# Performance work log

Measured on AMD Instinct MI355X. Metric: run time of the kernel, lower is better.

## Reference

```python
import jax, jax.numpy as jnp
import numpy as np

B, L, E = 256, 500, 300  # bsz, max_doc_len, word_embed_dim
KS = [3, 5, 7]           # filters_size


def setup_inputs() -> dict:
    key = jax.random.key(0)
    ks = jax.random.split(key, 1 + 2 * len(KS))
    inp = {"x": jax.random.normal(ks[0], (B, L, E), jnp.float32)}
    i = 1
    for k in KS:
        # PyTorch Conv2d default init scale ~ 1/sqrt(fan_in)
        inp[f"aw{k}"] = jax.random.normal(ks[i], (k, E), jnp.float32) / np.sqrt(k * E).astype(np.float32); i += 1
        inp[f"ab{k}"] = jnp.zeros((1,), jnp.float32)
        inp[f"cw{k}"] = jax.random.normal(ks[i], (E,), jnp.float32) / np.sqrt(E).astype(np.float32); i += 1
        inp[f"cb{k}"] = jnpp = jnp.zeros((1,), jnp.float32)
    return inp


def _branch(x, aw, ab, cw, cb):
    # x: (B, L, E); aw: (k, E); cw: (E,)
    k = aw.shape[0]
    p = (k - 1) // 2
    x4 = x[:, None, :, :]            # NCHW: (B, 1, L, E)
    w4 = aw[None, None, :, :]        # OIHW: (1, 1, k, E)
    s = jax.lax.conv_general_dilated(x4, w4, window_strides=(1, 1),
                                     padding=((p, p), (0, 0)))  # (B, 1, L, 1)
    score = jax.nn.sigmoid(s + ab[0])[:, 0, :, :]               # (B, L, 1)
    gated = x * score                                           # broadcast over E
    # Conv2d(1,1,(1,E)) == per-timestep dot product over E
    return jnp.tanh(jnp.einsum('ble,e->bl', gated, cw) + cb[0])  # (B, L)


def reference(x, aw3, ab3, cw3, cb3, aw5, ab5, cw5, cb5, aw7, ab7, cw7, cb7):
    return (_branch(x, aw3, ab3, cw3, cb3),
            _branch(x, aw5, ab5, cw5, cb5),
            _branch(x, aw7, ab7, cw7, cb7))
```

## Files before the change

### kernel.cpp

```cpp
#include <hip/hip_runtime.h>
#include <math.h>

#define BB 256
#define LL 500
#define EE 300
#define NROWS (BB * LL)
#define NJ 18
#define NC 75
#define TOUT 56
#define NTILE 9
#define DROWS 64

__global__ __launch_bounds__(256) void fused_kernel(
    const float* __restrict__ x,
    const float* __restrict__ aw3, const float* __restrict__ ab3,
    const float* __restrict__ cw3, const float* __restrict__ cb3,
    const float* __restrict__ aw5, const float* __restrict__ ab5,
    const float* __restrict__ cw5, const float* __restrict__ cb5,
    const float* __restrict__ aw7, const float* __restrict__ ab7,
    const float* __restrict__ cw7, const float* __restrict__ cb7,
    float* __restrict__ out)
{
    __shared__ float4 wlds[NJ * NC];
    __shared__ float dlds[DROWS][NJ + 1];

    const int tid = threadIdx.x;

    {
        const float4* s3a = (const float4*)aw3;
        const float4* s3c = (const float4*)cw3;
        const float4* s5a = (const float4*)aw5;
        const float4* s5c = (const float4*)cw5;
        const float4* s7a = (const float4*)aw7;
        const float4* s7c = (const float4*)cw7;
        for (int i = tid; i < 225; i += 256) wlds[i]        = s3a[i];
        for (int i = tid; i < 75;  i += 256) wlds[225 + i]  = s3c[i];
        for (int i = tid; i < 375; i += 256) wlds[300 + i]  = s5a[i];
        for (int i = tid; i < 75;  i += 256) wlds[675 + i]  = s5c[i];
        for (int i = tid; i < 525; i += 256) wlds[750 + i]  = s7a[i];
        for (int i = tid; i < 75;  i += 256) wlds[1275 + i] = s7c[i];
    }

    const int b    = blockIdx.x / NTILE;
    const int t    = blockIdx.x % NTILE;
    const int l0   = t * TOUT - 3;
    const int wave = tid >> 6;
    const int lane = tid & 63;
    const int g    = lane >> 4;
    const int j    = lane & 15;
    const int lr   = wave * 16 + g * 4;

    bool valid[4];
    const float4* xr[4];
#pragma unroll
    for (int rr = 0; rr < 4; ++rr) {
        const int l = l0 + lr + rr;
        valid[rr] = (l >= 0) && (l < LL);
        const int lc = l < 0 ? 0 : (l >= LL ? LL - 1 : l);
        xr[rr] = (const float4*)(x + ((size_t)b * LL + lc) * EE);
    }

    float4 xall[5][4];
#pragma unroll
    for (int k = 0; k < 5; ++k) {
        const int c = (k == 4) ? ((j < 11) ? (j + 64) : 74) : (j + 16 * k);
#pragma unroll
        for (int rr = 0; rr < 4; ++rr) xall[k][rr] = xr[rr][c];
    }

    __syncthreads();

    float acc[NJ][4];
#pragma unroll
    for (int d = 0; d < NJ; ++d)
#pragma unroll
        for (int rr = 0; rr < 4; ++rr) acc[d][rr] = 0.0f;

#define COMPUTE(k, c)                                                               \
    {                                                                               \
        _Pragma("unroll")                                                           \
        for (int d = 0; d < NJ; ++d) {                                              \
            const float4 w = wlds[d * NC + (c)];                                    \
            acc[d][0] = fmaf(xall[k][0].w, w.w, fmaf(xall[k][0].z, w.z, fmaf(xall[k][0].y, w.y, fmaf(xall[k][0].x, w.x, acc[d][0])))); \
            acc[d][1] = fmaf(xall[k][1].w, w.w, fmaf(xall[k][1].z, w.z, fmaf(xall[k][1].y, w.y, fmaf(xall[k][1].x, w.x, acc[d][1])))); \
            acc[d][2] = fmaf(xall[k][2].w, w.w, fmaf(xall[k][2].z, w.z, fmaf(xall[k][2].y, w.y, fmaf(xall[k][2].x, w.x, acc[d][2])))); \
            acc[d][3] = fmaf(xall[k][3].w, w.w, fmaf(xall[k][3].z, w.z, fmaf(xall[k][3].y, w.y, fmaf(xall[k][3].x, w.x, acc[d][3])))); \
        }                                                                           \
    }

    COMPUTE(0, j)
    COMPUTE(1, j + 16)
    COMPUTE(2, j + 32)
    COMPUTE(3, j + 48)
    if (j < 11) {
        COMPUTE(4, j + 64)
    }
#undef COMPUTE

#pragma unroll
    for (int d = 0; d < NJ; ++d)
#pragma unroll
        for (int rr = 0; rr < 4; ++rr) {
            float v = acc[d][rr];
            v += __shfl_xor(v, 1, 16);
            v += __shfl_xor(v, 2, 16);
            v += __shfl_xor(v, 4, 16);
            v += __shfl_xor(v, 8, 16);
            acc[d][rr] = v;
        }

#pragma unroll
    for (int rr = 0; rr < 4; ++rr) {
        if (j == rr) {
            const float vf = valid[rr] ? 1.0f : 0.0f;
#pragma unroll
            for (int d = 0; d < NJ; ++d) dlds[lr + rr][d] = acc[d][rr] * vf;
        }
    }

    __syncthreads();

    if (wave < 3 && lane < TOUT) {
        const int lo = t * TOUT + lane;
        if (lo < LL) {
            const int c = lane + 3;
            const int r = b * LL + lo;

            if (wave == 0) {
                float pre = 0.0f;
#pragma unroll
                for (int tp = 0; tp < 3; ++tp) pre += dlds[c + tp - 1][tp];
                const float s = 1.0f / (1.0f + expf(-(pre + ab3[0])));
                out[r] = tanhf(s * dlds[c][3] + cb3[0]);
            } else if (wave == 1) {
                float pre = 0.0f;
#pragma unroll
                for (int tp = 0; tp < 5; ++tp) pre += dlds[c + tp - 2][4 + tp];
                const float s = 1.0f / (1.0f + expf(-(pre + ab5[0])));
                out[NROWS + r] = tanhf(s * dlds[c][9] + cb5[0]);
            } else {
                float pre = 0.0f;
#pragma unroll
                for (int tp = 0; tp < 7; ++tp) pre += dlds[c + tp - 3][10 + tp];
                const float s = 1.0f / (1.0f + expf(-(pre + ab7[0])));
                out[2 * NROWS + r] = tanhf(s * dlds[c][17] + cb7[0]);
            }
        }
    }
}

extern "C" void kernel_launch(void* const* d_in, const int* in_sizes, int n_in,
                              void* d_out, int out_size, void* d_ws, size_t ws_size,
                              hipStream_t stream) {
    const float* x   = (const float*)d_in[0];
    const float* aw3 = (const float*)d_in[1];
    const float* ab3 = (const float*)d_in[2];
    const float* cw3 = (const float*)d_in[3];
    const float* cb3 = (const float*)d_in[4];
    const float* aw5 = (const float*)d_in[5];
    const float* ab5 = (const float*)d_in[6];
    const float* cw5 = (const float*)d_in[7];
    const float* cb5 = (const float*)d_in[8];
    const float* aw7 = (const float*)d_in[9];
    const float* ab7 = (const float*)d_in[10];
    const float* cw7 = (const float*)d_in[11];
    const float* cb7 = (const float*)d_in[12];

    float* out = (float*)d_out;

    fused_kernel<<<BB * NTILE, 256, 0, stream>>>(
        x, aw3, ab3, cw3, cb3, aw5, ab5, cw5, cb5, aw7, ab7, cw7, cb7, out);
}
```

Measured before the change: 258.4 us.

## Stage x through double-buffered LDS in E-chunks with larger row tiles

Replaces the per-block register load of a 56-row tile with a 250-row tile per block (2 blocks per batch). x is streamed through a double-buffered shared-memory buffer in 5-float4 E-chunks, with the next chunk prefetched into registers while the current one is computed. Each thread now accumulates 9 dot products for 2 rows directly, which removes the cross-lane shuffle reductions and cuts halo reloads from 9 tiles to 2. The cost is a grid of only 512 blocks and a barrier on every chunk iteration.

```diff
diff --git a/kernel.cpp b/kernel.cpp
--- a/kernel.cpp
+++ b/kernel.cpp
@@ -7,9 +7,11 @@
 #define NROWS (BB * LL)
 #define NJ 18
 #define NC 75
-#define TOUT 56
-#define NTILE 9
-#define DROWS 64
+#define CB 5
+#define NB 15
+#define DR 256
+#define TOUT 250
+#define XB4 (DR * CB)
 
 __global__ __launch_bounds__(256) void fused_kernel(
     const float* __restrict__ x,
@@ -22,9 +24,28 @@
     float* __restrict__ out)
 {
     __shared__ float4 wlds[NJ * NC];
-    __shared__ float dlds[DROWS][NJ + 1];
+    __shared__ float4 xbuf[2][XB4];
+    float* dlds = (float*)&xbuf[0][0];
 
     const int tid = threadIdx.x;
+    const int b   = blockIdx.x >> 1;
+    const int t   = blockIdx.x & 1;
+    const int l0  = t * TOUT - 3;
+
+    const float4* xp[5];
+#pragma unroll
+    for (int q = 0; q < 5; ++q) {
+        const int L   = q * 256 + tid;
+        const int row = L / CB;
+        const int cc  = L - row * CB;
+        int g = l0 + row;
+        g = g < 0 ? 0 : (g >= LL ? LL - 1 : g);
+        xp[q] = (const float4*)(x + ((size_t)b * LL + g) * EE) + cc;
+    }
+
+    float4 xn[5];
+#pragma unroll
+    for (int q = 0; q < 5; ++q) xn[q] = xp[q][0];
 
     {
         const float4* s3a = (const float4*)aw3;
@@ -41,110 +62,83 @@
         for (int i = tid; i < 75;  i += 256) wlds[1275 + i] = s7c[i];
     }
 
-    const int b    = blockIdx.x / NTILE;
-    const int t    = blockIdx.x % NTILE;
-    const int l0   = t * TOUT - 3;
-    const int wave = tid >> 6;
-    const int lane = tid & 63;
-    const int g    = lane >> 4;
-    const int j    = lane & 15;
-    const int lr   = wave * 16 + g * 4;
-
-    bool valid[4];
-    const float4* xr[4];
 #pragma unroll
-    for (int rr = 0; rr < 4; ++rr) {
-        const int l = l0 + lr + rr;
-        valid[rr] = (l >= 0) && (l < LL);
-        const int lc = l < 0 ? 0 : (l >= LL ? LL - 1 : l);
-        xr[rr] = (const float4*)(x + ((size_t)b * LL + lc) * EE);
-    }
-
-    float4 xall[5][4];
-#pragma unroll
-    for (int k = 0; k < 5; ++k) {
-        const int c = (k == 4) ? ((j < 11) ? (j + 64) : 74) : (j + 16 * k);
-#pragma unroll
-        for (int rr = 0; rr < 4; ++rr) xall[k][rr] = xr[rr][c];
-    }
+    for (int q = 0; q < 5; ++q) xbuf[0][q * 256 + tid] = xn[q];
 
     __syncthreads();
 
-    float acc[NJ][4];
+    const int wav   = tid >> 6;
+    const int lane  = tid & 63;
+    const int dbase = (wav >> 1) * 9;
+    const int rbase = (wav & 1) * 128 + lane;
+
+    float vf0, vf1;
+    { const int g0 = l0 + rbase;      vf0 = (g0 >= 0 && g0 < LL) ? 1.0f : 0.0f; }
+    { const int g1 = l0 + rbase + 64; vf1 = (g1 >= 0 && g1 < LL) ? 1.0f : 0.0f; }
+
+    float acc[9][2];
 #pragma unroll
-    for (int d = 0; d < NJ; ++d)
+    for (int dd = 0; dd < 9; ++dd) { acc[dd][0] = 0.0f; acc[dd][1] = 0.0f; }
+
+#pragma unroll 1
+    for (int s = 0; s < NB; ++s) {
+        if (s < NB - 1) {
 #pragma unroll
-        for (int rr = 0; rr < 4; ++rr) acc[d][rr] = 0.0f;
+            for (int q = 0; q < 5; ++q) { xp[q] += CB; xn[q] = xp[q][0]; }
+        }
 
-#define COMPUTE(k, c)                                                               \
-    {                                                                               \
-        _Pragma("unroll")                                                           \
-        for (int d = 0; d < NJ; ++d) {                                              \
-            const float4 w = wlds[d * NC + (c)];                                    \
-            acc[d][0] = fmaf(xall[k][0].w, w.w, fmaf(xall[k][0].z, w.z, fmaf(xall[k][0].y, w.y, fmaf(xall[k][0].x, w.x, acc[d][0])))); \
-            acc[d][1] = fmaf(xall[k][1].w, w.w, fmaf(xall[k][1].z, w.z, fmaf(xall[k][1].y, w.y, fmaf(xall[k][1].x, w.x, acc[d][1])))); \
-            acc[d][2] = fmaf(xall[k][2].w, w.w, fmaf(xall[k][2].z, w.z, fmaf(xall[k][2].y, w.y, fmaf(xall[k][2].x, w.x, acc[d][2])))); \
-            acc[d][3] = fmaf(xall[k][3].w, w.w, fmaf(xall[k][3].z, w.z, fmaf(xall[k][3].y, w.y, fmaf(xall[k][3].x, w.x, acc[d][3])))); \
-        }                                                                           \
+        const float4* xb = &xbuf[s & 1][rbase * CB];
+        const float4* wb = &wlds[dbase * NC + s * CB];
+
+#pragma unroll
+        for (int cc = 0; cc < CB; ++cc) {
+            const float4 x0 = xb[cc];
+            const float4 x1 = xb[64 * CB + cc];
+#pragma unroll
+            for (int dd = 0; dd < 9; ++dd) {
+                const float4 w = wb[dd * NC + cc];
+                acc[dd][0] = fmaf(x0.w, w.w, fmaf(x0.z, w.z, fmaf(x0.y, w.y, fmaf(x0.x, w.x, acc[dd][0]))));
+                acc[dd][1] = fmaf(x1.w, w.w, fmaf(x1.z, w.z, fmaf(x1.y, w.y, fmaf(x1.x, w.x, acc[dd][1]))));
+            }
+        }
+
+        if (s < NB - 1) {
+#pragma unroll
+            for (int q = 0; q < 5; ++q) xbuf[(s + 1) & 1][q * 256 + tid] = xn[q];
+        }
+        __syncthreads();
     }
 
-    COMPUTE(0, j)
-    COMPUTE(1, j + 16)
-    COMPUTE(2, j + 32)
-    COMPUTE(3, j + 48)
-    if (j < 11) {
-        COMPUTE(4, j + 64)
+#pragma unroll
+    for (int dd = 0; dd < 9; ++dd) {
+        dlds[rbase * (NJ + 1) + dbase + dd]        = acc[dd][0] * vf0;
+        dlds[(rbase + 64) * (NJ + 1) + dbase + dd] = acc[dd][1] * vf1;
     }
-#undef COMPUTE
-
-#pragma unroll
-    for (int d = 0; d < NJ; ++d)
-#pragma unroll
-        for (int rr = 0; rr < 4; ++rr) {
-            float v = acc[d][rr];
-            v += __shfl_xor(v, 1, 16);
-            v += __shfl_xor(v, 2, 16);
-            v += __shfl_xor(v, 4, 16);
-            v += __shfl_xor(v, 8, 16);
-            acc[d][rr] = v;
-        }
-
-#pragma unroll
-    for (int rr = 0; rr < 4; ++rr) {
-        if (j == rr) {
-            const float vf = valid[rr] ? 1.0f : 0.0f;
-#pragma unroll
-            for (int d = 0; d < NJ; ++d) dlds[lr + rr][d] = acc[d][rr] * vf;
-        }
-    }
-
     __syncthreads();
 
-    if (wave < 3 && lane < TOUT) {
-        const int lo = t * TOUT + lane;
-        if (lo < LL) {
-            const int c = lane + 3;
-            const int r = b * LL + lo;
-
-            if (wave == 0) {
-                float pre = 0.0f;
+    if (tid < TOUT) {
+        const int c = tid + 3;
+        const int r = b * LL + t * TOUT + tid;
+        {
+            float pre = 0.0f;
 #pragma unroll
-                for (int tp = 0; tp < 3; ++tp) pre += dlds[c + tp - 1][tp];
-                const float s = 1.0f / (1.0f + expf(-(pre + ab3[0])));
-                out[r] = tanhf(s * dlds[c][3] + cb3[0]);
-            } else if (wave == 1) {
-                float pre = 0.0f;
+            for (int tp = 0; tp < 3; ++tp) pre += dlds[(c + tp - 1) * (NJ + 1) + tp];
+            const float sg = 1.0f / (1.0f + expf(-(pre + ab3[0])));
+            out[r] = tanhf(sg * dlds[c * (NJ + 1) + 3] + cb3[0]);
+        }
+        {
+            float pre = 0.0f;
 #pragma unroll
-                for (int tp = 0; tp < 5; ++tp) pre += dlds[c + tp - 2][4 + tp];
-                const float s = 1.0f / (1.0f + expf(-(pre + ab5[0])));
-                out[NROWS + r] = tanhf(s * dlds[c][9] + cb5[0]);
-            } else {
-                float pre = 0.0f;
+            for (int tp = 0; tp < 5; ++tp) pre += dlds[(c + tp - 2) * (NJ + 1) + 4 + tp];
+            const float sg = 1.0f / (1.0f + expf(-(pre + ab5[0])));
+            out[NROWS + r] = tanhf(sg * dlds[c * (NJ + 1) + 9] + cb5[0]);
+        }
+        {
+            float pre = 0.0f;
 #pragma unroll
-                for (int tp = 0; tp < 7; ++tp) pre += dlds[c + tp - 3][10 + tp];
-                const float s = 1.0f / (1.0f + expf(-(pre + ab7[0])));
-                out[2 * NROWS + r] = tanhf(s * dlds[c][17] + cb7[0]);
-            }
+            for (int tp = 0; tp < 7; ++tp) pre += dlds[(c + tp - 3) * (NJ + 1) + 10 + tp];
+            const float sg = 1.0f / (1.0f + expf(-(pre + ab7[0])));
+            out[2 * NROWS + r] = tanhf(sg * dlds[c * (NJ + 1) + 17] + cb7[0]);
         }
     }
 }
@@ -168,6 +162,6 @@
 
     float* out = (float*)d_out;
 
-    fused_kernel<<<BB * NTILE, 256, 0, stream>>>(
+    fused_kernel<<<BB * 2, 256, 0, stream>>>(
         x, aw3, ab3, cw3, cb3, aw5, ab5, cw5, cb5, aw7, ab7, cw7, cb7, out);
 }
```

Result: slower. 292.3 us (+13.1%).

## Process three tiles per block with register prefetch and DPP reductions

Applied to the files above, without the earlier changes.

Each block now handles three consecutive sequence tiles instead of one, which cuts the grid from 2304 to 768 blocks and loads the weight table into LDS once per three tiles. While the current tile is being reduced and written, the next tile's x rows are prefetched into registers. The shuffle-based 16-lane reduction is replaced with DPP row operations, and custom waitcnt+barrier fences replace __syncthreads. Risks are fewer blocks for latency hiding, higher register pressure from the prefetch, and an extra barrier per tile.

```diff
diff --git a/kernel.cpp b/kernel.cpp
--- a/kernel.cpp
+++ b/kernel.cpp
@@ -8,8 +8,29 @@
 #define NJ 18
 #define NC 75
 #define TOUT 56
-#define NTILE 9
+#define GRP 3
+#define NT 3
 #define DROWS 64
+
+
+__device__ __forceinline__ float red16(float v) {
+    int t;
+    t = __builtin_amdgcn_update_dpp(0, __float_as_int(v), 0xB1, 0xF, 0xF, true);
+    v += __int_as_float(t);
+    t = __builtin_amdgcn_update_dpp(0, __float_as_int(v), 0x4E, 0xF, 0xF, true);
+    v += __int_as_float(t);
+    t = __builtin_amdgcn_update_dpp(0, __float_as_int(v), 0x124, 0xF, 0xF, true);
+    v += __int_as_float(t);
+    t = __builtin_amdgcn_update_dpp(0, __float_as_int(v), 0x128, 0xF, 0xF, true);
+    v += __int_as_float(t);
+    return v;
+}
+
+__device__ __forceinline__ void lds_fence_barrier() {
+    asm volatile("s_waitcnt lgkmcnt(0)" ::: "memory");
+    __builtin_amdgcn_s_barrier();
+    asm volatile("" ::: "memory");
+}
 
 __global__ __launch_bounds__(256) void fused_kernel(
     const float* __restrict__ x,
@@ -41,40 +62,51 @@
         for (int i = tid; i < 75;  i += 256) wlds[1275 + i] = s7c[i];
     }
 
-    const int b    = blockIdx.x / NTILE;
-    const int t    = blockIdx.x % NTILE;
-    const int l0   = t * TOUT - 3;
+    const int b    = blockIdx.x / GRP;
+    const int grp  = blockIdx.x % GRP;
     const int wave = tid >> 6;
     const int lane = tid & 63;
     const int g    = lane >> 4;
     const int j    = lane & 15;
     const int lr   = wave * 16 + g * 4;
 
-    bool valid[4];
-    const float4* xr[4];
-#pragma unroll
-    for (int rr = 0; rr < 4; ++rr) {
-        const int l = l0 + lr + rr;
-        valid[rr] = (l >= 0) && (l < LL);
-        const int lc = l < 0 ? 0 : (l >= LL ? LL - 1 : l);
-        xr[rr] = (const float4*)(x + ((size_t)b * LL + lc) * EE);
-    }
+    const float* xbb = x + (size_t)b * LL * EE;
 
     float4 xall[5][4];
-#pragma unroll
-    for (int k = 0; k < 5; ++k) {
-        const int c = (k == 4) ? ((j < 11) ? (j + 64) : 74) : (j + 16 * k);
-#pragma unroll
-        for (int rr = 0; rr < 4; ++rr) xall[k][rr] = xr[rr][c];
-    }
-
-    __syncthreads();
-
-    float acc[NJ][4];
-#pragma unroll
-    for (int d = 0; d < NJ; ++d)
-#pragma unroll
-        for (int rr = 0; rr < 4; ++rr) acc[d][rr] = 0.0f;
+    {
+        const int l0 = (grp * NT) * TOUT - 3;
+#pragma unroll
+        for (int rr = 0; rr < 4; ++rr) {
+            const int l  = l0 + lr + rr;
+            const int lc = l < 0 ? 0 : (l >= LL ? LL - 1 : l);
+            const float4* xr = (const float4*)(xbb + (size_t)lc * EE);
+#pragma unroll
+            for (int k = 0; k < 5; ++k) {
+                const int c = (k == 4) ? ((j < 11) ? (j + 64) : 74) : (j + 16 * k);
+                xall[k][rr] = xr[c];
+            }
+        }
+    }
+
+    lds_fence_barrier();
+
+#pragma unroll 1
+    for (int tt = 0; tt < NT; ++tt) {
+        const int t  = grp * NT + tt;
+        const int l0 = t * TOUT - 3;
+
+        float vf[4];
+#pragma unroll
+        for (int rr = 0; rr < 4; ++rr) {
+            const int l = l0 + lr + rr;
+            vf[rr] = (l >= 0 && l < LL) ? 1.0f : 0.0f;
+        }
+
+        float acc[NJ][4];
+#pragma unroll
+        for (int d = 0; d < NJ; ++d)
+#pragma unroll
+            for (int rr = 0; rr < 4; ++rr) acc[d][rr] = 0.0f;
 
 #define COMPUTE(k, c)                                                               \
     {                                                                               \
@@ -88,64 +120,74 @@
         }                                                                           \
     }
 
-    COMPUTE(0, j)
-    COMPUTE(1, j + 16)
-    COMPUTE(2, j + 32)
-    COMPUTE(3, j + 48)
-    if (j < 11) {
-        COMPUTE(4, j + 64)
-    }
+        COMPUTE(0, j)
+        COMPUTE(1, j + 16)
+        COMPUTE(2, j + 32)
+        COMPUTE(3, j + 48)
+        if (j < 11) {
+            COMPUTE(4, j + 64)
+        }
 #undef COMPUTE
 
-#pragma unroll
-    for (int d = 0; d < NJ; ++d)
+        if (tt + 1 < NT) {
+            const int l0n = (t + 1) * TOUT - 3;
+#pragma unroll
+            for (int rr = 0; rr < 4; ++rr) {
+                const int l  = l0n + lr + rr;
+                const int lc = l < 0 ? 0 : (l >= LL ? LL - 1 : l);
+                const float4* xr = (const float4*)(xbb + (size_t)lc * EE);
+#pragma unroll
+                for (int k = 0; k < 5; ++k) {
+                    const int c = (k == 4) ? ((j < 11) ? (j + 64) : 74) : (j + 16 * k);
+                    xall[k][rr] = xr[c];
+                }
+            }
+        }
+
+#pragma unroll
+        for (int d = 0; d < NJ; ++d)
+#pragma unroll
+            for (int rr = 0; rr < 4; ++rr) acc[d][rr] = red16(acc[d][rr]);
+
 #pragma unroll
         for (int rr = 0; rr < 4; ++rr) {
-            float v = acc[d][rr];
-            v += __shfl_xor(v, 1, 16);
-            v += __shfl_xor(v, 2, 16);
-            v += __shfl_xor(v, 4, 16);
-            v += __shfl_xor(v, 8, 16);
-            acc[d][rr] = v;
-        }
-
-#pragma unroll
-    for (int rr = 0; rr < 4; ++rr) {
-        if (j == rr) {
-            const float vf = valid[rr] ? 1.0f : 0.0f;
-#pragma unroll
-            for (int d = 0; d < NJ; ++d) dlds[lr + rr][d] = acc[d][rr] * vf;
-        }
-    }
-
-    __syncthreads();
-
-    if (wave < 3 && lane < TOUT) {
-        const int lo = t * TOUT + lane;
-        if (lo < LL) {
-            const int c = lane + 3;
-            const int r = b * LL + lo;
-
-            if (wave == 0) {
-                float pre = 0.0f;
-#pragma unroll
-                for (int tp = 0; tp < 3; ++tp) pre += dlds[c + tp - 1][tp];
-                const float s = 1.0f / (1.0f + expf(-(pre + ab3[0])));
-                out[r] = tanhf(s * dlds[c][3] + cb3[0]);
-            } else if (wave == 1) {
-                float pre = 0.0f;
-#pragma unroll
-                for (int tp = 0; tp < 5; ++tp) pre += dlds[c + tp - 2][4 + tp];
-                const float s = 1.0f / (1.0f + expf(-(pre + ab5[0])));
-                out[NROWS + r] = tanhf(s * dlds[c][9] + cb5[0]);
-            } else {
-                float pre = 0.0f;
-#pragma unroll
-                for (int tp = 0; tp < 7; ++tp) pre += dlds[c + tp - 3][10 + tp];
-                const float s = 1.0f / (1.0f + expf(-(pre + ab7[0])));
-                out[2 * NROWS + r] = tanhf(s * dlds[c][17] + cb7[0]);
-            }
-        }
+            if (j == rr) {
+#pragma unroll
+                for (int d = 0; d < NJ; ++d) dlds[lr + rr][d] = acc[d][rr] * vf[rr];
+            }
+        }
+
+        lds_fence_barrier();
+
+        if (wave < 3 && lane < TOUT) {
+            const int lo = t * TOUT + lane;
+            if (lo < LL) {
+                const int c = lane + 3;
+                const int r = b * LL + lo;
+
+                if (wave == 0) {
+                    float pre = 0.0f;
+#pragma unroll
+                    for (int tp = 0; tp < 3; ++tp) pre += dlds[c + tp - 1][tp];
+                    const float s = 1.0f / (1.0f + expf(-(pre + ab3[0])));
+                    out[r] = tanhf(s * dlds[c][3] + cb3[0]);
+                } else if (wave == 1) {
+                    float pre = 0.0f;
+#pragma unroll
+                    for (int tp = 0; tp < 5; ++tp) pre += dlds[c + tp - 2][4 + tp];
+                    const float s = 1.0f / (1.0f + expf(-(pre + ab5[0])));
+                    out[NROWS + r] = tanhf(s * dlds[c][9] + cb5[0]);
+                } else {
+                    float pre = 0.0f;
+#pragma unroll
+                    for (int tp = 0; tp < 7; ++tp) pre += dlds[c + tp - 3][10 + tp];
+                    const float s = 1.0f / (1.0f + expf(-(pre + ab7[0])));
+                    out[2 * NROWS + r] = tanhf(s * dlds[c][17] + cb7[0]);
+                }
+            }
+        }
+
+        lds_fence_barrier();
     }
 }
 
@@ -168,6 +210,6 @@
 
     float* out = (float*)d_out;
 
-    fused_kernel<<<BB * NTILE, 256, 0, stream>>>(
+    fused_kernel<<<BB * GRP, 256, 0, stream>>>(
         x, aw3, ab3, cw3, cb3, aw5, ab5, cw5, cb5, aw7, ab7, cw7, cb7, out);
 }
```

New measurement: 246.7 us. 4.5% less time.

## Stream x chunks through rotating registers, use DPP reductions and LDS-only barriers

Applied to the files above, without the earlier changes.

Global loads of x are now issued in three rotating float4 register buffers, interleaved with the FMA blocks, instead of loading all five chunks up front. The barrier after the weight copy waits only on LDS counters, so those loads can stay in flight across it. The 16-lane butterfly reductions use DPP quad_perm and row_ror moves instead of __shfl_xor, which avoids LDS permute traffic. Together these aim to cut register pressure and hide global-load latency, but they depend on hand-written waitcnt and barrier semantics and on the compiler scheduling the loads well.

```diff
diff --git a/kernel.cpp b/kernel.cpp
--- a/kernel.cpp
+++ b/kernel.cpp
@@ -10,6 +10,26 @@
 #define TOUT 56
 #define NTILE 9
 #define DROWS 64
+
+
+__device__ __forceinline__ float red16(float v) {
+    int t;
+    t = __builtin_amdgcn_update_dpp(0, __float_as_int(v), 0xB1, 0xF, 0xF, true);
+    v += __int_as_float(t);
+    t = __builtin_amdgcn_update_dpp(0, __float_as_int(v), 0x4E, 0xF, 0xF, true);
+    v += __int_as_float(t);
+    t = __builtin_amdgcn_update_dpp(0, __float_as_int(v), 0x124, 0xF, 0xF, true);
+    v += __int_as_float(t);
+    t = __builtin_amdgcn_update_dpp(0, __float_as_int(v), 0x128, 0xF, 0xF, true);
+    v += __int_as_float(t);
+    return v;
+}
+
+__device__ __forceinline__ void lds_fence_barrier() {
+    asm volatile("s_waitcnt lgkmcnt(0)" ::: "memory");
+    __builtin_amdgcn_s_barrier();
+    asm volatile("" ::: "memory");
+}
 
 __global__ __launch_bounds__(256) void fused_kernel(
     const float* __restrict__ x,
@@ -60,15 +80,18 @@
         xr[rr] = (const float4*)(x + ((size_t)b * LL + lc) * EE);
     }
 
-    float4 xall[5][4];
-#pragma unroll
-    for (int k = 0; k < 5; ++k) {
-        const int c = (k == 4) ? ((j < 11) ? (j + 64) : 74) : (j + 16 * k);
-#pragma unroll
-        for (int rr = 0; rr < 4; ++rr) xall[k][rr] = xr[rr][c];
+#define LOADC(buf, k)                                                       \
+    {                                                                       \
+        const int c = ((k) == 4) ? ((j < 11) ? (j + 64) : 74) : (j + 16 * (k)); \
+        _Pragma("unroll")                                                   \
+        for (int rr = 0; rr < 4; ++rr) buf[rr] = xr[rr][c];                 \
     }
 
-    __syncthreads();
+    float4 xc0[4], xc1[4], xc2[4];
+    LOADC(xc0, 0)
+    LOADC(xc1, 1)
+
+    lds_fence_barrier();
 
     float acc[NJ][4];
 #pragma unroll
@@ -76,38 +99,35 @@
 #pragma unroll
         for (int rr = 0; rr < 4; ++rr) acc[d][rr] = 0.0f;
 
-#define COMPUTE(k, c)                                                               \
+#define COMP(buf, c)                                                                \
     {                                                                               \
         _Pragma("unroll")                                                           \
         for (int d = 0; d < NJ; ++d) {                                              \
             const float4 w = wlds[d * NC + (c)];                                    \
-            acc[d][0] = fmaf(xall[k][0].w, w.w, fmaf(xall[k][0].z, w.z, fmaf(xall[k][0].y, w.y, fmaf(xall[k][0].x, w.x, acc[d][0])))); \
-            acc[d][1] = fmaf(xall[k][1].w, w.w, fmaf(xall[k][1].z, w.z, fmaf(xall[k][1].y, w.y, fmaf(xall[k][1].x, w.x, acc[d][1])))); \
-            acc[d][2] = fmaf(xall[k][2].w, w.w, fmaf(xall[k][2].z, w.z, fmaf(xall[k][2].y, w.y, fmaf(xall[k][2].x, w.x, acc[d][2])))); \
-            acc[d][3] = fmaf(xall[k][3].w, w.w, fmaf(xall[k][3].z, w.z, fmaf(xall[k][3].y, w.y, fmaf(xall[k][3].x, w.x, acc[d][3])))); \
+            acc[d][0] = fmaf(buf[0].w, w.w, fmaf(buf[0].z, w.z, fmaf(buf[0].y, w.y, fmaf(buf[0].x, w.x, acc[d][0])))); \
+            acc[d][1] = fmaf(buf[1].w, w.w, fmaf(buf[1].z, w.z, fmaf(buf[1].y, w.y, fmaf(buf[1].x, w.x, acc[d][1])))); \
+            acc[d][2] = fmaf(buf[2].w, w.w, fmaf(buf[2].z, w.z, fmaf(buf[2].y, w.y, fmaf(buf[2].x, w.x, acc[d][2])))); \
+            acc[d][3] = fmaf(buf[3].w, w.w, fmaf(buf[3].z, w.z, fmaf(buf[3].y, w.y, fmaf(buf[3].x, w.x, acc[d][3])))); \
         }                                                                           \
     }
 
-    COMPUTE(0, j)
-    COMPUTE(1, j + 16)
-    COMPUTE(2, j + 32)
-    COMPUTE(3, j + 48)
+    COMP(xc0, j)
+    LOADC(xc2, 2)
+    COMP(xc1, j + 16)
+    LOADC(xc0, 3)
+    COMP(xc2, j + 32)
+    LOADC(xc1, 4)
+    COMP(xc0, j + 48)
     if (j < 11) {
-        COMPUTE(4, j + 64)
+        COMP(xc1, j + 64)
     }
-#undef COMPUTE
+#undef COMP
+#undef LOADC
 
 #pragma unroll
     for (int d = 0; d < NJ; ++d)
 #pragma unroll
-        for (int rr = 0; rr < 4; ++rr) {
-            float v = acc[d][rr];
-            v += __shfl_xor(v, 1, 16);
-            v += __shfl_xor(v, 2, 16);
-            v += __shfl_xor(v, 4, 16);
-            v += __shfl_xor(v, 8, 16);
-            acc[d][rr] = v;
-        }
+        for (int rr = 0; rr < 4; ++rr) acc[d][rr] = red16(acc[d][rr]);
 
 #pragma unroll
     for (int rr = 0; rr < 4; ++rr) {
@@ -118,7 +138,7 @@
         }
     }
 
-    __syncthreads();
+    lds_fence_barrier();
 
     if (wave < 3 && lane < TOUT) {
         const int lo = t * TOUT + lane;
```

New measurement: 246.8 us. -4.5%, faster.
